# Kernel optimization log

Measured on AMD Instinct MI355X. Metric: run time of the kernel, lower is better.

The kernel has to match this reference:

```python
import jax, jax.numpy as jnp
import numpy as np

TEMPERATURE = 0.5
EPS = 1e-8  # torch CosineSimilarity default eps


def setup_inputs() -> dict:
    key = jax.random.key(0)
    k1, k2 = jax.random.split(key)
    B, D = 4096, 256
    z_i = jax.random.normal(k1, (B, D), dtype=jnp.float32)
    z_j = jax.random.normal(k2, (B, D), dtype=jnp.float32)
    return {"z_i": z_i, "z_j": z_j}


def _normalize(x):
    # torch cosine_similarity clamps each norm at eps
    n = jnp.maximum(jnp.linalg.norm(x, axis=-1, keepdims=True), EPS)
    return x / n


def reference(z_i, z_j):
    B = z_i.shape[0]
    z = jnp.concatenate([z_i, z_j], axis=0)            # [2B, D]
    zn = _normalize(z)                                  # [2B, D]
    sim = jnp.einsum('id,jd->ij', zn, zn) / TEMPERATURE  # [2B, 2B]
    sim_exp = jnp.exp(sim)
    mask = jnp.eye(2 * B, dtype=bool)
    sim_sum = jnp.sum(jnp.where(mask, 0.0, sim_exp), axis=1)  # [2B]
    # positive pair similarity, computed on original (unconcatenated) pairs
    zi_n = _normalize(z_i)
    zj_n = _normalize(z_j)
    pos = jnp.exp(jnp.sum(zi_n * zj_n, axis=-1) / TEMPERATURE)  # [B]
    pos = jnp.concatenate([pos, pos], axis=0)          # [2B]
    loss = -jnp.log(pos / sim_sum)
    return jnp.mean(loss)
```

## Files before the change

kernel.cpp:

```cpp
#include <hip/hip_runtime.h>
#include <hip/hip_bf16.h>
#include <stdint.h>


#define BROWS 4096
#define DIM   256
#define N2    8192

typedef __attribute__((ext_vector_type(4))) float          f32x4;
typedef __attribute__((ext_vector_type(8))) short          s16x8;
typedef __attribute__((ext_vector_type(4))) unsigned short u16x4;

#define S_EXP  1.6986436597467051f
#define LN2    0.6931471805599453f

__device__ inline unsigned short f2bf(float f) {
    uint32_t b = __float_as_uint(f);
    b += 0x7fffu + ((b >> 16) & 1u);
    return (unsigned short)(b >> 16);
}
__device__ inline float bf2f(unsigned short u) {
    return __uint_as_float(((uint32_t)u) << 16);
}

__device__ inline void gload_lds16(const void* g, void* l) {
    __builtin_amdgcn_global_load_lds(
        (const __attribute__((address_space(1))) uint32_t*)g,
        (__attribute__((address_space(3))) uint32_t*)l, 16, 0, 0);
}

__device__ inline float wave_reduce(float v) {
    #pragma unroll
    for (int m = 1; m < 64; m <<= 1) v += __shfl_xor(v, m);
    return v;
}

__global__ __launch_bounds__(256) void k_norm_pos(const float* __restrict__ zi,
                                                  const float* __restrict__ zj,
                                                  unsigned short* __restrict__ zn,
                                                  float* __restrict__ diag,
                                                  float* __restrict__ posv,
                                                  unsigned int* __restrict__ counter) {
    if (blockIdx.x == 0 && threadIdx.x == 0) *counter = 0u;
    int i    = blockIdx.x * 4 + (threadIdx.x >> 6);
    int lane = threadIdx.x & 63;
    f32x4 a = *(const f32x4*)(zi + (size_t)i * DIM + lane * 4);
    f32x4 b = *(const f32x4*)(zj + (size_t)i * DIM + lane * 4);
    float ssa = a[0]*a[0] + a[1]*a[1] + a[2]*a[2] + a[3]*a[3];
    float ssb = b[0]*b[0] + b[1]*b[1] + b[2]*b[2] + b[3]*b[3];
    float dab = a[0]*b[0] + a[1]*b[1] + a[2]*b[2] + a[3]*b[3];
    ssa = wave_reduce(ssa);
    ssb = wave_reduce(ssb);
    dab = wave_reduce(dab);
    float na = 1.0f / fmaxf(sqrtf(ssa), 1e-8f);
    float nb = 1.0f / fmaxf(sqrtf(ssb), 1e-8f);
    if (lane == 0) posv[i] = 2.0f * dab * na * nb;

    float sa = na * S_EXP, sb = nb * S_EXP;
    u16x4 oa, ob;
    float da = 0.0f, db = 0.0f;
    #pragma unroll
    for (int k = 0; k < 4; ++k) {
        unsigned short ua = f2bf(a[k] * sa);
        unsigned short ub = f2bf(b[k] * sb);
        oa[k] = ua; ob[k] = ub;
        float fa = bf2f(ua), fb = bf2f(ub);
        da += fa * fa; db += fb * fb;
    }
    *(u16x4*)(zn + (size_t)i * DIM + lane * 4)           = oa;
    *(u16x4*)(zn + (size_t)(i + BROWS) * DIM + lane * 4) = ob;
    da = wave_reduce(da);
    db = wave_reduce(db);
    if (lane == 0) { diag[i] = da; diag[i + BROWS] = db; }
}

__global__ __launch_bounds__(256, 2) void k_simsum(const unsigned short* __restrict__ zn,
                                                   float* __restrict__ partial) {
    __shared__ unsigned short lds[2][64 * DIM];
    int bid = blockIdx.x;
    int rb = bid & 31;
    int cc = bid >> 5;
    int rowbase = rb * 256;
    int colbase = cc * 512;
    int tid = threadIdx.x, lane = tid & 63, w = tid >> 6;
    int cl = lane & 15, g = lane >> 4;

    s16x8 afrag[4][8];
    #pragma unroll
    for (int rt = 0; rt < 4; ++rt) {
        int row = rowbase + w * 64 + rt * 16 + cl;
        const unsigned short* ap = zn + (size_t)row * DIM + g * 8;
        #pragma unroll
        for (int kc = 0; kc < 8; ++kc)
            afrag[rt][kc] = *(const s16x8*)(ap + kc * 32);
    }

    float pp[4][4];
    #pragma unroll
    for (int rt = 0; rt < 4; ++rt)
        #pragma unroll
        for (int r = 0; r < 4; ++r) pp[rt][r] = 0.0f;

    auto stage = [&](int buf, int s) {
        int crow = colbase + s * 64 + lane;
        const unsigned short* gsrc = zn + (size_t)crow * DIM;
        char* base = (char*)&lds[buf][0];
        #pragma unroll
        for (int i = 0; i < 8; ++i)
            gload_lds16(gsrc + i * 32 + w * 8, base + i * 4096 + w * 1024);
    };

    stage(0, 0);
    __syncthreads();

    for (int s = 0; s < 8; ++s) {
        int cur = s & 1;
        if (s < 7) stage(cur ^ 1, s + 1);

        const char* lbase = (const char*)&lds[cur][0];
        #pragma unroll
        for (int ct = 0; ct < 4; ++ct) {
            f32x4 acc[4];
            #pragma unroll
            for (int rt = 0; rt < 4; ++rt) acc[rt] = (f32x4){0.f, 0.f, 0.f, 0.f};
            #pragma unroll
            for (int kc = 0; kc < 8; ++kc) {
                s16x8 bfrag = *(const s16x8*)(lbase + kc * 4096 + g * 1024 +
                                              (ct * 16 + cl) * 16);
                #pragma unroll
                for (int rt = 0; rt < 4; ++rt)
                    acc[rt] = __builtin_amdgcn_mfma_f32_16x16x32_bf16(
                                  afrag[rt][kc], bfrag, acc[rt], 0, 0, 0);
            }
            #pragma unroll
            for (int rt = 0; rt < 4; ++rt)
                #pragma unroll
                for (int r = 0; r < 4; ++r)
                    pp[rt][r] += __builtin_amdgcn_exp2f(acc[rt][r]);
        }
        __syncthreads();
    }

    #pragma unroll
    for (int rt = 0; rt < 4; ++rt) {
        #pragma unroll
        for (int r = 0; r < 4; ++r) {
            float v = pp[rt][r];
            v += __shfl_xor(v, 1);
            v += __shfl_xor(v, 2);
            v += __shfl_xor(v, 4);
            v += __shfl_xor(v, 8);
            if (cl == 0)
                partial[(size_t)cc * N2 + rowbase + w * 64 + rt * 16 + g * 4 + r] = v;
        }
    }
}

__global__ __launch_bounds__(256) void k_loss(const float* __restrict__ partial,
                                              const float* __restrict__ diag,
                                              const float* __restrict__ posv,
                                              float* __restrict__ blocksum,
                                              unsigned int* __restrict__ counter,
                                              float* __restrict__ out) {
    int row = blockIdx.x * 256 + threadIdx.x;
    float sum = 0.0f;
    #pragma unroll
    for (int c = 0; c < 16; ++c) sum += partial[(size_t)c * N2 + row];
    sum -= __builtin_amdgcn_exp2f(diag[row]);
    float lr = __builtin_amdgcn_logf(sum) * LN2 - posv[row & (BROWS - 1)];
    lr = wave_reduce(lr);
    __shared__ float red[4];
    if ((threadIdx.x & 63) == 0) red[threadIdx.x >> 6] = lr;
    __syncthreads();
    if (threadIdx.x == 0) {
        blocksum[blockIdx.x] = red[0] + red[1] + red[2] + red[3];
        __threadfence();
        unsigned int old = atomicAdd(counter, 1u);
        if (old == 31u) {
            __threadfence();
            volatile const float* bs = blocksum;
            float t = 0.0f;
            for (int i = 0; i < 32; ++i) t += bs[i];
            out[0] = t * (1.0f / N2);
        }
    }
}

extern "C" void kernel_launch(void* const* d_in, const int* in_sizes, int n_in,
                              void* d_out, int out_size, void* d_ws, size_t ws_size,
                              hipStream_t stream) {
    const float* zi = (const float*)d_in[0];
    const float* zj = (const float*)d_in[1];
    float* out = (float*)d_out;

    char* ws = (char*)d_ws;
    unsigned short* zn    = (unsigned short*)ws;
    float* diag           = (float*)(ws + (4u << 20));
    float* posv           = (float*)(ws + (4u << 20) + (32u << 10));
    float* blocksum       = (float*)(ws + (4u << 20) + (48u << 10));
    unsigned int* counter = (unsigned int*)(ws + (4u << 20) + (52u << 10));
    float* partial        = (float*)(ws + (4u << 20) + (64u << 10));

    k_norm_pos<<<BROWS / 4, 256, 0, stream>>>(zi, zj, zn, diag, posv, counter);
    k_simsum<<<512, 256, 0, stream>>>(zn, partial);
    k_loss<<<32, 256, 0, stream>>>(partial, diag, posv, blocksum, counter, out);
}
```

Baseline: 53.14 us.

## Exploit similarity matrix symmetry by computing only upper-triangular tiles

Switches the similarity-sum kernel from a full 32x16 grid of 256x512 tiles to 528 blocks of 256x256 tiles covering only the upper triangle (diagonal plus off-diagonal pairs). Off-diagonal tiles also emit column sums of exp values through a small LDS reduction, so each tile contributes to both its row block and its column block. This roughly halves the MFMA and exp work in exchange for extra shuffles, LDS traffic, a sync-dependent store per stage, and a loss kernel that now reads 32 partial slices instead of 16.

Result: slower. 58.69 us (+10.4%).

```diff
diff --git a/kernel.cpp b/kernel.cpp
--- a/kernel.cpp
+++ b/kernel.cpp
@@ -77,11 +77,23 @@
 __global__ __launch_bounds__(256, 2) void k_simsum(const unsigned short* __restrict__ zn,
                                                    float* __restrict__ partial) {
     __shared__ unsigned short lds[2][64 * DIM];
+    __shared__ float ldsC[2][4][64];
+
     int bid = blockIdx.x;
-    int rb = bid & 31;
-    int cc = bid >> 5;
-    int rowbase = rb * 256;
-    int colbase = cc * 512;
+    int a, b;
+    if (bid < 32) {
+        a = bid; b = bid;
+    } else {
+        int k = bid - 32;
+        a = (int)((63.0f - sqrtf(3969.0f - 8.0f * (float)k)) * 0.5f);
+        if (a < 0) a = 0; if (a > 30) a = 30;
+        while ((a + 1) * (62 - a) / 2 <= k) ++a;
+        while (a * (63 - a) / 2 > k) --a;
+        b = k - a * (63 - a) / 2 + a + 1;
+    }
+    bool offdiag = (a != b);
+    int rowbase = a * 256;
+    int colbase = b * 256;
     int tid = threadIdx.x, lane = tid & 63, w = tid >> 6;
     int cl = lane & 15, g = lane >> 4;
 
@@ -113,9 +125,9 @@
     stage(0, 0);
     __syncthreads();
 
-    for (int s = 0; s < 8; ++s) {
+    for (int s = 0; s < 4; ++s) {
         int cur = s & 1;
-        if (s < 7) stage(cur ^ 1, s + 1);
+        if (s < 3) stage(cur ^ 1, s + 1);
 
         const char* lbase = (const char*)&lds[cur][0];
         #pragma unroll
@@ -132,13 +144,26 @@
                     acc[rt] = __builtin_amdgcn_mfma_f32_16x16x32_bf16(
                                   afrag[rt][kc], bfrag, acc[rt], 0, 0, 0);
             }
+            float ce = 0.0f;
             #pragma unroll
             for (int rt = 0; rt < 4; ++rt)
                 #pragma unroll
-                for (int r = 0; r < 4; ++r)
-                    pp[rt][r] += __builtin_amdgcn_exp2f(acc[rt][r]);
+                for (int r = 0; r < 4; ++r) {
+                    float e = __builtin_amdgcn_exp2f(acc[rt][r]);
+                    pp[rt][r] += e;
+                    ce += e;
+                }
+            ce += __shfl_xor(ce, 16);
+            ce += __shfl_xor(ce, 32);
+            if (lane < 16) ldsC[cur][w][ct * 16 + lane] = ce;
         }
         __syncthreads();
+
+        if (offdiag && tid < 64) {
+            float cs = ldsC[cur][0][tid] + ldsC[cur][1][tid] +
+                       ldsC[cur][2][tid] + ldsC[cur][3][tid];
+            partial[(size_t)a * N2 + colbase + s * 64 + tid] = cs;
+        }
     }
 
     #pragma unroll
@@ -151,7 +176,7 @@
             v += __shfl_xor(v, 4);
             v += __shfl_xor(v, 8);
             if (cl == 0)
-                partial[(size_t)cc * N2 + rowbase + w * 64 + rt * 16 + g * 4 + r] = v;
+                partial[(size_t)b * N2 + rowbase + w * 64 + rt * 16 + g * 4 + r] = v;
         }
     }
 }
@@ -165,7 +190,7 @@
     int row = blockIdx.x * 256 + threadIdx.x;
     float sum = 0.0f;
     #pragma unroll
-    for (int c = 0; c < 16; ++c) sum += partial[(size_t)c * N2 + row];
+    for (int c = 0; c < 32; ++c) sum += partial[(size_t)c * N2 + row];
     sum -= __builtin_amdgcn_exp2f(diag[row]);
     float lr = __builtin_amdgcn_logf(sum) * LN2 - posv[row & (BROWS - 1)];
     lr = wave_reduce(lr);
@@ -202,6 +227,6 @@
     float* partial        = (float*)(ws + (4u << 20) + (64u << 10));
 
     k_norm_pos<<<BROWS / 4, 256, 0, stream>>>(zi, zj, zn, diag, posv, counter);
-    k_simsum<<<512, 256, 0, stream>>>(zn, partial);
+    k_simsum<<<528, 256, 0, stream>>>(zn, partial);
     k_loss<<<32, 256, 0, stream>>>(partial, diag, posv, blocksum, counter, out);
 }
```
